# Kernel tuning notes

Hardware: AMD Instinct MI355X
Metric: run time of the kernel (lower is better)

The kernel has to match this reference:

```python
import jax, jax.numpy as jnp
import numpy as np

DEPTH = 10
NUM_FEATURES = 512
NUM_LEAVES = 2 ** DEPTH
TEMPERATURE = 0.1
BATCH = 32768


def _leaf_codes():
    # codes[leaf, i] = bit i (MSB first) of leaf index
    leaves = np.arange(NUM_LEAVES)
    shifts = DEPTH - 1 - np.arange(DEPTH)
    codes = (leaves[:, None] >> shifts[None, :]) & 1
    return jnp.asarray(codes, dtype=jnp.float32)  # [num_leaves, depth]


def setup_inputs() -> dict:
    key = jax.random.key(0)
    k1, k2, k3 = jax.random.split(key, 3)
    x = jax.random.normal(k1, (BATCH, NUM_FEATURES), dtype=jnp.float32)
    feature_weights = jax.random.normal(k2, (DEPTH, NUM_FEATURES), dtype=jnp.float32) * 0.01
    thresholds = jnp.zeros((DEPTH,), dtype=jnp.float32)
    leaf_values = jax.random.normal(k3, (NUM_FEATURES, NUM_LEAVES), dtype=jnp.float32) * 0.01
    return {"x": x, "feature_weights": feature_weights,
            "thresholds": thresholds, "leaf_values": leaf_values}


def reference(x, feature_weights, thresholds, leaf_values):
    codes = _leaf_codes()                                   # [L, D]
    probs = jax.nn.softmax(feature_weights, axis=1)          # [D, F]
    sel = x @ probs.T                                        # [B, D]
    decisions = jax.nn.sigmoid((sel - thresholds) / TEMPERATURE)  # [B, D]
    # leaf_probs[b, l] = prod_d (p*code + (1-p)*(1-code))
    p = decisions[:, None, :]                                # [B, 1, D]
    c = codes[None, :, :]                                    # [1, L, D]
    leaf_probs = jnp.prod(p * c + (1.0 - p) * (1.0 - c), axis=-1)  # [B, L]
    out = leaf_probs @ leaf_values.T                         # [B, F]
    return out
```

## Files before the change

kernel.cpp:

```cpp
#include <hip/hip_runtime.h>
#include <hip/hip_bf16.h>
#include <cstdint>

using u16 = unsigned short;
using u32 = unsigned int;

#define DEPTH 10
#define NF 512
#define NL 1024
#define BATCH_N 32768
#define TEMP_INV 10.0f
#define GBM 64
#define GBK 32
#define NSTEP (NL / GBK)

typedef float f32x4 __attribute__((ext_vector_type(4)));
typedef short s16x8 __attribute__((ext_vector_type(8)));
typedef __bf16 bf16x8 __attribute__((ext_vector_type(8)));
typedef __bf16 bf16x4 __attribute__((ext_vector_type(4)));

__device__ __forceinline__ u16 f2bf(float f) {
  u32 u = __float_as_uint(f);
  u = (u + 0x7fffu + ((u >> 16) & 1u)) >> 16;
  return (u16)u;
}

__device__ __forceinline__ void gld_lds16(const void* g, void* lds) {
  __builtin_amdgcn_global_load_lds(
      (const __attribute__((address_space(1))) void*)g,
      (__attribute__((address_space(3))) void*)lds, 16, 0, 0);
}

__global__ void k_softmax(const float* __restrict__ fw, float* __restrict__ probs) {
  int w = threadIdx.x >> 6;
  int lane = threadIdx.x & 63;
  if (w >= DEPTH) return;
  const float* row = fw + w * NF;
  float v[8];
  float mx = -1e30f;
#pragma unroll
  for (int i = 0; i < 8; ++i) { v[i] = row[lane * 8 + i]; mx = fmaxf(mx, v[i]); }
#pragma unroll
  for (int s = 32; s >= 1; s >>= 1) mx = fmaxf(mx, __shfl_xor(mx, s));
  float sum = 0.f;
#pragma unroll
  for (int i = 0; i < 8; ++i) { v[i] = __expf(v[i] - mx); sum += v[i]; }
#pragma unroll
  for (int s = 32; s >= 1; s >>= 1) sum += __shfl_xor(sum, s);
  float inv = 1.0f / sum;
#pragma unroll
  for (int i = 0; i < 8; ++i) probs[w * NF + lane * 8 + i] = v[i] * inv;
}

__global__ void k_cvt(const float* __restrict__ lv, u16* __restrict__ lvb) {
  int i = (blockIdx.x * blockDim.x + threadIdx.x) * 8;
  float4 a = *(const float4*)(lv + i);
  float4 b = *(const float4*)(lv + i + 4);
  uint4 u;
  u.x = f2bf(a.x) | ((u32)f2bf(a.y) << 16);
  u.y = f2bf(a.z) | ((u32)f2bf(a.w) << 16);
  u.z = f2bf(b.x) | ((u32)f2bf(b.y) << 16);
  u.w = f2bf(b.z) | ((u32)f2bf(b.w) << 16);
  *(uint4*)(lvb + i) = u;
}

__global__ __launch_bounds__(512, 4) void k_fused(const float* __restrict__ x,
                                                  const float* __restrict__ probs,
                                                  const float* __restrict__ thr,
                                                  const u16* __restrict__ B,
                                                  float* __restrict__ C) {
  __shared__ char smem[73728];
  u16* const As = (u16*)smem;
  u16* const Bs = (u16*)(smem + 8192);
  float* const Ps = (float*)(smem + 40960);

  const int tid = threadIdx.x;
  const int lane = tid & 63;
  const int w = tid >> 6;
  const int brow = blockIdx.x * GBM;
  const int row = tid >> 3;
  const int q = tid & 7;

  for (int i = tid; i < DEPTH * NF; i += 512) Ps[i] = probs[i];
  __syncthreads();

  float selacc[DEPTH];
#pragma unroll
  for (int d = 0; d < DEPTH; ++d) selacc[d] = 0.f;
  const float* xr = x + (size_t)(brow + row) * NF + q * 4;
#pragma unroll
  for (int i = 0; i < 16; ++i) {
    float4 xv = *(const float4*)(xr + i * 32);
#pragma unroll
    for (int d = 0; d < DEPTH; ++d) {
      f32x4 pv = *(const f32x4*)&Ps[d * NF + i * 32 + q * 4];
      selacc[d] += xv.x * pv[0] + xv.y * pv[1] + xv.z * pv[2] + xv.w * pv[3];
    }
  }
  float p[DEPTH];
#pragma unroll
  for (int d = 0; d < DEPTH; ++d) {
    float s = selacc[d];
    s += __shfl_xor(s, 1);
    s += __shfl_xor(s, 2);
    s += __shfl_xor(s, 4);
    p[d] = 1.0f / (1.0f + __expf(-(s - thr[d]) * TEMP_INV));
  }
  const float f567 = ((q & 4) ? p[5] : 1.f - p[5]) *
                     ((q & 2) ? p[6] : 1.f - p[6]) *
                     ((q & 1) ? p[7] : 1.f - p[7]);
  const float t0 = f567 * (1.f - p[8]) * (1.f - p[9]);
  const float t1 = f567 * (1.f - p[8]) * p[9];
  const float t2 = f567 * p[8] * (1.f - p[9]);
  const float t3 = f567 * p[8] * p[9];
  const float p0a = 1.f - p[0], p0b = p[0];
  const float p1a = 1.f - p[1], p1b = p[1];
  const float p2a = 1.f - p[2], p2b = p[2];
  const float p3a = 1.f - p[3], p3b = p[3];
  const float p4a = 1.f - p[4], p4b = p[4];

  const int awb = row * 64 + (((q >> 1) ^ (row & 3)) << 4) + ((q & 1) << 3);

  f32x4 acc[4][4];
#pragma unroll
  for (int m = 0; m < 4; ++m)
#pragma unroll
    for (int n = 0; n < 4; ++n) acc[m][n] = {0.f, 0.f, 0.f, 0.f};

  auto STAGE = [&](int step, int buf) {
#pragma unroll
    for (int it = 0; it < 4; ++it) {
      int r = it * 128 + (tid >> 2);
      int sL = tid & 3;
      const u16* src = B + (size_t)r * NL + step * GBK + ((sL ^ (r & 3)) * 8);
      gld_lds16(src, (char*)Bs + buf * 32768 + (it * 512 + tid) * 16);
    }
  };
  auto GENA = [&](int step, int buf) {
    float base = ((step & 16) ? p0b : p0a) * ((step & 8) ? p1b : p1a);
    base *= ((step & 4) ? p2b : p2a);
    base *= ((step & 2) ? p3b : p3a);
    base *= ((step & 1) ? p4b : p4a);
    bf16x4 v;
    v[0] = (__bf16)(base * t0);
    v[1] = (__bf16)(base * t1);
    v[2] = (__bf16)(base * t2);
    v[3] = (__bf16)(base * t3);
    *(bf16x4*)((char*)As + buf * 4096 + awb) = v;
  };

  STAGE(0, 0);
  GENA(0, 0);
  asm volatile("s_waitcnt vmcnt(0) lgkmcnt(0)" ::: "memory");
  __builtin_amdgcn_s_barrier();

  const int rA = lane & 15;
  const int sg = lane >> 4;
  const int aoff = rA * 64 + ((sg ^ (rA & 3)) << 4);
  const int boff = (w * 64 + rA) * 64 + ((sg ^ (rA & 3)) << 4);

  for (int kk = 0; kk < NSTEP; ++kk) {
    const int cur = kk & 1;
    if (kk + 1 < NSTEP) {
      STAGE(kk + 1, cur ^ 1);
      GENA(kk + 1, cur ^ 1);
    }
    const char* ab = (const char*)As + cur * 4096;
    const char* bb = (const char*)Bs + cur * 32768;
    bf16x8 a0 = __builtin_bit_cast(bf16x8, *(const s16x8*)(ab + aoff));
    bf16x8 a1 = __builtin_bit_cast(bf16x8, *(const s16x8*)(ab + aoff + 1024));
    bf16x8 a2 = __builtin_bit_cast(bf16x8, *(const s16x8*)(ab + aoff + 2048));
    bf16x8 a3 = __builtin_bit_cast(bf16x8, *(const s16x8*)(ab + aoff + 3072));
#pragma unroll
    for (int n = 0; n < 4; ++n) {
      bf16x8 bn = __builtin_bit_cast(bf16x8, *(const s16x8*)(bb + boff + n * 1024));
      acc[0][n] = __builtin_amdgcn_mfma_f32_16x16x32_bf16(a0, bn, acc[0][n], 0, 0, 0);
      acc[1][n] = __builtin_amdgcn_mfma_f32_16x16x32_bf16(a1, bn, acc[1][n], 0, 0, 0);
      acc[2][n] = __builtin_amdgcn_mfma_f32_16x16x32_bf16(a2, bn, acc[2][n], 0, 0, 0);
      acc[3][n] = __builtin_amdgcn_mfma_f32_16x16x32_bf16(a3, bn, acc[3][n], 0, 0, 0);
    }
    asm volatile("s_waitcnt vmcnt(0) lgkmcnt(0)" ::: "memory");
    __builtin_amdgcn_s_barrier();
  }

  const int c0 = lane & 15;
  const int r0 = (lane >> 4) * 4;
#pragma unroll
  for (int m = 0; m < 4; ++m)
#pragma unroll
    for (int n = 0; n < 4; ++n) {
      int col = w * 64 + n * 16 + c0;
#pragma unroll
      for (int r = 0; r < 4; ++r)
        C[(size_t)(brow + m * 16 + r0 + r) * NF + col] = acc[m][n][r];
    }
}

extern "C" void kernel_launch(void* const* d_in, const int* in_sizes, int n_in,
                              void* d_out, int out_size, void* d_ws, size_t ws_size,
                              hipStream_t stream) {
  const float* x  = (const float*)d_in[0];
  const float* fw = (const float*)d_in[1];
  const float* th = (const float*)d_in[2];
  const float* lv = (const float*)d_in[3];
  float* out = (float*)d_out;

  float* probs = (float*)d_ws;
  u16* lvb = (u16*)((char*)d_ws + DEPTH * NF * 4);

  k_softmax<<<1, 640, 0, stream>>>(fw, probs);
  k_cvt<<<(NF * NL / 8) / 256, 256, 0, stream>>>(lv, lvb);
  k_fused<<<BATCH_N / GBM, 512, 0, stream>>>(x, probs, th, lvb, out);
}
```

Measured before the change: 70.14 us.

## Split decision computation into separate kernel and retile GEMM to 128x256 blocks

Moves the x·probsᵀ selection and sigmoid into a standalone kernel that writes per-row decisions to workspace. The GEMM kernel now uses 128x256 output tiles with 4 waves in a 2x2 layout, each wave holding 4x8 MFMA accumulators, and builds leaf-probability A tiles from the precomputed decisions. This raises arithmetic intensity per staged B tile and cuts shared memory per block, at the cost of an extra launch and a round trip of the decisions through global memory. The 64x512 tiles and 512-thread blocks are replaced.

```diff
diff --git a/kernel.cpp b/kernel.cpp
--- a/kernel.cpp
+++ b/kernel.cpp
@@ -10,14 +10,14 @@
 #define NL 1024
 #define BATCH_N 32768
 #define TEMP_INV 10.0f
-#define GBM 64
+#define GBM 128
+#define GBN 256
 #define GBK 32
-#define NSTEP (NL / GBK)
+#define NSTEP 32
 
 typedef float f32x4 __attribute__((ext_vector_type(4)));
 typedef short s16x8 __attribute__((ext_vector_type(8)));
 typedef __bf16 bf16x8 __attribute__((ext_vector_type(8)));
-typedef __bf16 bf16x4 __attribute__((ext_vector_type(4)));
 
 __device__ __forceinline__ u16 f2bf(float f) {
   u32 u = __float_as_uint(f);
@@ -64,89 +64,105 @@
   *(uint4*)(lvb + i) = u;
 }
 
-__global__ __launch_bounds__(512, 4) void k_fused(const float* __restrict__ x,
-                                                  const float* __restrict__ probs,
-                                                  const float* __restrict__ thr,
-                                                  const u16* __restrict__ B,
-                                                  float* __restrict__ C) {
-  __shared__ char smem[73728];
-  u16* const As = (u16*)smem;
-  u16* const Bs = (u16*)(smem + 8192);
-  float* const Ps = (float*)(smem + 40960);
-
+__global__ __launch_bounds__(256) void k_sel(const float* __restrict__ x,
+                                             const float* __restrict__ probs,
+                                             const float* __restrict__ thr,
+                                             float* __restrict__ pout) {
+  __shared__ float Ps[DEPTH * NF];
+  const int tid = threadIdx.x;
+  for (int i = tid; i < DEPTH * NF; i += 256) Ps[i] = probs[i];
+  __syncthreads();
+  const int q = tid & 7;
+  const int row = blockIdx.x * 32 + (tid >> 3);
+  const float* xr = x + (size_t)row * NF + q * 4;
+  float acc[DEPTH];
+#pragma unroll
+  for (int d = 0; d < DEPTH; ++d) acc[d] = 0.f;
+#pragma unroll
+  for (int i = 0; i < 16; ++i) {
+    float4 xv = *(const float4*)(xr + i * 32);
+#pragma unroll
+    for (int d = 0; d < DEPTH; ++d) {
+      f32x4 pv = *(const f32x4*)&Ps[d * NF + i * 32 + q * 4];
+      acc[d] += xv.x * pv[0] + xv.y * pv[1] + xv.z * pv[2] + xv.w * pv[3];
+    }
+  }
+#pragma unroll
+  for (int d = 0; d < DEPTH; ++d) {
+    float s = acc[d];
+    s += __shfl_xor(s, 1);
+    s += __shfl_xor(s, 2);
+    s += __shfl_xor(s, 4);
+    float pd = 1.0f / (1.0f + __expf(-(s - thr[d]) * TEMP_INV));
+    if (q == (d & 7)) pout[(size_t)row * DEPTH + d] = pd;
+  }
+}
+
+__global__ __launch_bounds__(256, 2) void k_gemm(const u16* __restrict__ B,
+                                                 const float* __restrict__ p,
+                                                 float* __restrict__ C) {
+  __shared__ char smem[49152];
   const int tid = threadIdx.x;
   const int lane = tid & 63;
   const int w = tid >> 6;
-  const int brow = blockIdx.x * GBM;
-  const int row = tid >> 3;
-  const int q = tid & 7;
-
-  for (int i = tid; i < DEPTH * NF; i += 512) Ps[i] = probs[i];
-  __syncthreads();
-
-  float selacc[DEPTH];
-#pragma unroll
-  for (int d = 0; d < DEPTH; ++d) selacc[d] = 0.f;
-  const float* xr = x + (size_t)(brow + row) * NF + q * 4;
-#pragma unroll
-  for (int i = 0; i < 16; ++i) {
-    float4 xv = *(const float4*)(xr + i * 32);
-#pragma unroll
-    for (int d = 0; d < DEPTH; ++d) {
-      f32x4 pv = *(const f32x4*)&Ps[d * NF + i * 32 + q * 4];
-      selacc[d] += xv.x * pv[0] + xv.y * pv[1] + xv.z * pv[2] + xv.w * pv[3];
-    }
-  }
-  float p[DEPTH];
-#pragma unroll
-  for (int d = 0; d < DEPTH; ++d) {
-    float s = selacc[d];
-    s += __shfl_xor(s, 1);
-    s += __shfl_xor(s, 2);
-    s += __shfl_xor(s, 4);
-    p[d] = 1.0f / (1.0f + __expf(-(s - thr[d]) * TEMP_INV));
-  }
-  const float f567 = ((q & 4) ? p[5] : 1.f - p[5]) *
-                     ((q & 2) ? p[6] : 1.f - p[6]) *
-                     ((q & 1) ? p[7] : 1.f - p[7]);
-  const float t0 = f567 * (1.f - p[8]) * (1.f - p[9]);
-  const float t1 = f567 * (1.f - p[8]) * p[9];
-  const float t2 = f567 * p[8] * (1.f - p[9]);
-  const float t3 = f567 * p[8] * p[9];
-  const float p0a = 1.f - p[0], p0b = p[0];
-  const float p1a = 1.f - p[1], p1b = p[1];
-  const float p2a = 1.f - p[2], p2b = p[2];
-  const float p3a = 1.f - p[3], p3b = p[3];
-  const float p4a = 1.f - p[4], p4b = p[4];
-
-  const int awb = row * 64 + (((q >> 1) ^ (row & 3)) << 4) + ((q & 1) << 3);
-
-  f32x4 acc[4][4];
+  const int wm = w >> 1, wn = w & 1;
+  const int bm = blockIdx.x >> 1, bn = blockIdx.x & 1;
+  const int brow = bm * GBM, bcol = bn * GBN;
+
+  const int gr = tid >> 1;
+  const int gh = tid & 1;
+  const float* prw = p + (size_t)(brow + gr) * DEPTH;
+  float pv[10];
+#pragma unroll
+  for (int d = 0; d < 10; ++d) pv[d] = prw[d];
+  float T[16];
+  {
+    float s5 = gh ? pv[5] : 1.f - pv[5];
+    float a6 = 1.f - pv[6], b6 = pv[6], a7 = 1.f - pv[7], b7 = pv[7];
+    float a8 = 1.f - pv[8], b8 = pv[8], a9 = 1.f - pv[9], b9 = pv[9];
+    float m67[4] = {a6 * a7, a6 * b7, b6 * a7, b6 * b7};
+    float m89[4] = {a8 * a9, a8 * b9, b8 * a9, b8 * b9};
+#pragma unroll
+    for (int i = 0; i < 16; ++i) T[i] = s5 * m67[i >> 2] * m89[i & 3];
+  }
+  const float p0a = 1.f - pv[0], p0b = pv[0], p1a = 1.f - pv[1], p1b = pv[1],
+              p2a = 1.f - pv[2], p2b = pv[2], p3a = 1.f - pv[3], p3b = pv[3],
+              p4a = 1.f - pv[4], p4b = pv[4];
+
+  const int xorg = (gr >> 1) & 3;
+  const int wb0 = gr * 64 + (((gh * 2)     ^ xorg) << 4);
+  const int wb1 = gr * 64 + (((gh * 2 + 1) ^ xorg) << 4);
+
+  f32x4 acc[4][8];
 #pragma unroll
   for (int m = 0; m < 4; ++m)
 #pragma unroll
-    for (int n = 0; n < 4; ++n) acc[m][n] = {0.f, 0.f, 0.f, 0.f};
+    for (int n = 0; n < 8; ++n) acc[m][n] = {0.f, 0.f, 0.f, 0.f};
 
   auto STAGE = [&](int step, int buf) {
+    char* bsb = smem + 16384 + buf * 16384;
 #pragma unroll
     for (int it = 0; it < 4; ++it) {
-      int r = it * 128 + (tid >> 2);
-      int sL = tid & 3;
-      const u16* src = B + (size_t)r * NL + step * GBK + ((sL ^ (r & 3)) * 8);
-      gld_lds16(src, (char*)Bs + buf * 32768 + (it * 512 + tid) * 16);
+      int lin = it * 256 + tid;
+      int r = lin >> 2;
+      int slog = (lin & 3) ^ ((r >> 1) & 3);
+      gld_lds16(B + (size_t)(bcol + r) * NL + step * GBK + slog * 8, bsb + lin * 16);
     }
   };
   auto GENA = [&](int step, int buf) {
-    float base = ((step & 16) ? p0b : p0a) * ((step & 8) ? p1b : p1a);
-    base *= ((step & 4) ? p2b : p2a);
-    base *= ((step & 2) ? p3b : p3a);
-    base *= ((step & 1) ? p4b : p4a);
-    bf16x4 v;
-    v[0] = (__bf16)(base * t0);
-    v[1] = (__bf16)(base * t1);
-    v[2] = (__bf16)(base * t2);
-    v[3] = (__bf16)(base * t3);
-    *(bf16x4*)((char*)As + buf * 4096 + awb) = v;
+    float H = ((step & 16) ? p0b : p0a) * ((step & 8) ? p1b : p1a);
+    H *= (step & 4) ? p2b : p2a;
+    H *= (step & 2) ? p3b : p3a;
+    H *= (step & 1) ? p4b : p4a;
+    bf16x8 v0, v1;
+#pragma unroll
+    for (int j = 0; j < 8; ++j) {
+      v0[j] = (__bf16)(H * T[j]);
+      v1[j] = (__bf16)(H * T[8 + j]);
+    }
+    char* asb = smem + buf * 8192;
+    *(bf16x8*)(asb + wb0) = v0;
+    *(bf16x8*)(asb + wb1) = v1;
   };
 
   STAGE(0, 0);
@@ -154,10 +170,10 @@
   asm volatile("s_waitcnt vmcnt(0) lgkmcnt(0)" ::: "memory");
   __builtin_amdgcn_s_barrier();
 
-  const int rA = lane & 15;
-  const int sg = lane >> 4;
-  const int aoff = rA * 64 + ((sg ^ (rA & 3)) << 4);
-  const int boff = (w * 64 + rA) * 64 + ((sg ^ (rA & 3)) << 4);
+  const int rA = lane & 15, sg = lane >> 4;
+  const int soff = (sg ^ ((rA >> 1) & 3)) << 4;
+  const int aoff = (wm * 64 + rA) * 64 + soff;
+  const int boff = (wn * 128 + rA) * 64 + soff;
 
   for (int kk = 0; kk < NSTEP; ++kk) {
     const int cur = kk & 1;
@@ -165,19 +181,19 @@
       STAGE(kk + 1, cur ^ 1);
       GENA(kk + 1, cur ^ 1);
     }
-    const char* ab = (const char*)As + cur * 4096;
-    const char* bb = (const char*)Bs + cur * 32768;
-    bf16x8 a0 = __builtin_bit_cast(bf16x8, *(const s16x8*)(ab + aoff));
-    bf16x8 a1 = __builtin_bit_cast(bf16x8, *(const s16x8*)(ab + aoff + 1024));
-    bf16x8 a2 = __builtin_bit_cast(bf16x8, *(const s16x8*)(ab + aoff + 2048));
-    bf16x8 a3 = __builtin_bit_cast(bf16x8, *(const s16x8*)(ab + aoff + 3072));
-#pragma unroll
-    for (int n = 0; n < 4; ++n) {
-      bf16x8 bn = __builtin_bit_cast(bf16x8, *(const s16x8*)(bb + boff + n * 1024));
-      acc[0][n] = __builtin_amdgcn_mfma_f32_16x16x32_bf16(a0, bn, acc[0][n], 0, 0, 0);
-      acc[1][n] = __builtin_amdgcn_mfma_f32_16x16x32_bf16(a1, bn, acc[1][n], 0, 0, 0);
-      acc[2][n] = __builtin_amdgcn_mfma_f32_16x16x32_bf16(a2, bn, acc[2][n], 0, 0, 0);
-      acc[3][n] = __builtin_amdgcn_mfma_f32_16x16x32_bf16(a3, bn, acc[3][n], 0, 0, 0);
+    const char* ab = smem + cur * 8192;
+    const char* bb = smem + 16384 + cur * 16384;
+    bf16x8 a[4];
+#pragma unroll
+    for (int m = 0; m < 4; ++m)
+      a[m] = __builtin_bit_cast(bf16x8, *(const s16x8*)(ab + aoff + m * 1024));
+#pragma unroll
+    for (int n = 0; n < 8; ++n) {
+      bf16x8 bf = __builtin_bit_cast(bf16x8, *(const s16x8*)(bb + boff + n * 1024));
+      acc[0][n] = __builtin_amdgcn_mfma_f32_16x16x32_bf16(a[0], bf, acc[0][n], 0, 0, 0);
+      acc[1][n] = __builtin_amdgcn_mfma_f32_16x16x32_bf16(a[1], bf, acc[1][n], 0, 0, 0);
+      acc[2][n] = __builtin_amdgcn_mfma_f32_16x16x32_bf16(a[2], bf, acc[2][n], 0, 0, 0);
+      acc[3][n] = __builtin_amdgcn_mfma_f32_16x16x32_bf16(a[3], bf, acc[3][n], 0, 0, 0);
     }
     asm volatile("s_waitcnt vmcnt(0) lgkmcnt(0)" ::: "memory");
     __builtin_amdgcn_s_barrier();
@@ -188,11 +204,11 @@
 #pragma unroll
   for (int m = 0; m < 4; ++m)
 #pragma unroll
-    for (int n = 0; n < 4; ++n) {
-      int col = w * 64 + n * 16 + c0;
+    for (int n = 0; n < 8; ++n) {
+      int col = bcol + wn * 128 + n * 16 + c0;
 #pragma unroll
       for (int r = 0; r < 4; ++r)
-        C[(size_t)(brow + m * 16 + r0 + r) * NF + col] = acc[m][n][r];
+        C[(size_t)(brow + wm * 64 + m * 16 + r0 + r) * NF + col] = acc[m][n][r];
     }
 }
 
@@ -207,8 +223,10 @@
 
   float* probs = (float*)d_ws;
   u16* lvb = (u16*)((char*)d_ws + DEPTH * NF * 4);
+  float* pbuf = (float*)((char*)d_ws + DEPTH * NF * 4 + NF * NL * 2);
 
   k_softmax<<<1, 640, 0, stream>>>(fw, probs);
   k_cvt<<<(NF * NL / 8) / 256, 256, 0, stream>>>(lv, lvb);
-  k_fused<<<BATCH_N / GBM, 512, 0, stream>>>(x, probs, th, lvb, out);
-}
+  k_sel<<<BATCH_N / 32, 256, 0, stream>>>(x, probs, th, pbuf);
+  k_gemm<<<(BATCH_N / GBM) * 2, 256, 0, stream>>>(lvb, pbuf, out);
+}
```

Result: slower. 135.3 us (+92.8%).
